# Kernel tuning notes

Measured on AMD Instinct MI355X. Metric: run time of the kernel, lower is better.

## Reference

```python
import jax, jax.numpy as jnp
import numpy as np

N = 50000      # nodes
E = 800000     # edges
D = 200        # in_dim = hid_dim
R = 230        # num_rels
B = 100        # bdd bases -> submat = D // B = 2
S = D // B     # submatrix size (2)


def setup_inputs() -> dict:
    key = jax.random.key(0)
    ks = jax.random.split(key, 16)
    node_feat = jax.random.normal(ks[0], (N, D), dtype=jnp.float32)
    dynamic_emb = jax.random.normal(ks[1], (N, 1, D), dtype=jnp.float32)
    src = jax.random.randint(ks[2], (E,), 0, N, dtype=jnp.int32)
    dst = jax.random.randint(ks[3], (E,), 0, N, dtype=jnp.int32)
    etypes = jax.random.randint(ks[4], (E,), 0, R, dtype=jnp.int32)
    # BDD relational weights per layer: [R, B, S, S]
    w1 = jax.random.normal(ks[5], (R, B, S, S), dtype=jnp.float32) * 0.1
    loop_w1 = jax.random.normal(ks[6], (D, D), dtype=jnp.float32) * 0.05
    b1 = jnp.zeros((D,), dtype=jnp.float32)
    w2 = jax.random.normal(ks[7], (R, B, S, S), dtype=jnp.float32) * 0.1
    loop_w2 = jax.random.normal(ks[8], (D, D), dtype=jnp.float32) * 0.05
    b2 = jnp.zeros((D,), dtype=jnp.float32)
    # single-layer vanilla RNN (tanh) params
    W_ih = jax.random.normal(ks[9], (D, D), dtype=jnp.float32) * 0.05
    W_hh = jax.random.normal(ks[10], (D, D), dtype=jnp.float32) * 0.05
    b_ih = jnp.zeros((D,), dtype=jnp.float32)
    b_hh = jnp.zeros((D,), dtype=jnp.float32)
    return {"node_feat": node_feat, "dynamic_emb": dynamic_emb,
            "src": src, "dst": dst, "etypes": etypes,
            "w1": w1, "loop_w1": loop_w1, "b1": b1,
            "w2": w2, "loop_w2": loop_w2, "b2": b2,
            "W_ih": W_ih, "W_hh": W_hh, "b_ih": b_ih, "b_hh": b_hh}


def _rel_graph_conv_bdd(x, src, dst, etypes, edge_norm, w, loop_w, b):
    # gather source feats and apply per-edge-type block-diagonal transform
    xs = x[src].reshape(E, B, S)                     # [E, B, S]
    msg = jnp.einsum('ebi,ebio->ebo', xs, w[etypes]) # [E, B, S]
    msg = msg.reshape(E, D) * edge_norm              # edge-norm scaling
    agg = jax.ops.segment_sum(msg, dst, num_segments=N)  # scatter-add to dst
    return agg + x @ loop_w + b                      # self-loop + bias


def reference(node_feat, dynamic_emb, src, dst, etypes,
              w1, loop_w1, b1, w2, loop_w2, b2,
              W_ih, W_hh, b_ih, b_hh):
    # edge_norm = dst node norm = 1 / in-degree
    deg = jax.ops.segment_sum(jnp.ones((E,), jnp.float32), dst, num_segments=N)
    node_norm = jnp.where(deg > 0, 1.0 / jnp.maximum(deg, 1.0), 0.0)
    edge_norm = node_norm[dst][:, None]              # [E, 1]

    # RGCN layer 1 (tanh activation), layer 2 (no activation); dropout=eval
    h = _rel_graph_conv_bdd(node_feat, src, dst, etypes, edge_norm, w1, loop_w1, b1)
    h = jnp.tanh(h)
    h = _rel_graph_conv_bdd(h, src, dst, etypes, edge_norm, w2, loop_w2, b2)

    # single-step vanilla RNN: hn = tanh(x W_ih^T + b_ih + h0 W_hh^T + b_hh)
    h0 = dynamic_emb[:, 0, :]                        # [N, D]
    hn = jnp.tanh(h @ W_ih.T + b_ih + h0 @ W_hh.T + b_hh)
    return hn[:, None, :]                            # [N, 1, D]
```

## Files before the change

kernel.cpp:

```cpp
#include <hip/hip_runtime.h>

#define N_NODES 50000
#define N_EDGES 800000
#define DIM     200
#define NBLK    100
#define NRELS   230
#define NB_SCAN 196
#define KPAD    224
#define KPN     256
#define NROWPAD 50048
#define NFRAG8  (8 * 14 * 64)
#define EPADMAX (N_EDGES + 3 * N_NODES + 16)
#define DUMMYROW 50000

typedef __attribute__((ext_vector_type(8)))  short short8;
typedef __attribute__((ext_vector_type(16))) float f32x16;

__device__ __forceinline__ unsigned short f2bf(float f) {
    unsigned u = __float_as_uint(f);
    u += 0x7fffu + ((u >> 16) & 1u);
    return (unsigned short)(u >> 16);
}

__device__ __forceinline__ float bflo(unsigned u) { return __uint_as_float(u << 16); }
__device__ __forceinline__ float bfhi(unsigned u) { return __uint_as_float(u & 0xffff0000u); }
__device__ __forceinline__ float b2f(unsigned short u) { return __uint_as_float((unsigned)u << 16); }

__device__ __forceinline__ float tanh_fast(float x) {
    float xa = fminf(fmaxf(x, -15.0f), 15.0f);
    float e = __expf(2.0f * xa);
    return (e - 1.0f) / (e + 1.0f);
}

__device__ __forceinline__ int uread(int v, int l) {
    return __builtin_amdgcn_readlane(v, l);
}

#if __has_builtin(__builtin_amdgcn_fdot2_f32_bf16)
typedef __bf16 bf16x2 __attribute__((ext_vector_type(2)));
__device__ __forceinline__ float dot2bf(unsigned a, unsigned b, float c) {
    return __builtin_amdgcn_fdot2_f32_bf16(
        __builtin_bit_cast(bf16x2, a), __builtin_bit_cast(bf16x2, b), c, false);
}
#define CMP4(XU, WU)                                                    \
    { m0 = dot2bf(XU.x, WU.x, m0); m1 = dot2bf(XU.x, WU.y, m1);         \
      m2 = dot2bf(XU.y, WU.z, m2); m3 = dot2bf(XU.y, WU.w, m3); }
#else
#define CMP4(XU, WU)                                                    \
    { float x0 = bflo(XU.x), x1 = bfhi(XU.x);                           \
      float x2 = bflo(XU.y), x3 = bfhi(XU.y);                           \
      m0 += x0 * bflo(WU.x) + x1 * bfhi(WU.x);                          \
      m1 += x0 * bflo(WU.y) + x1 * bfhi(WU.y);                          \
      m2 += x2 * bflo(WU.z) + x3 * bfhi(WU.z);                          \
      m3 += x2 * bflo(WU.w) + x3 * bfhi(WU.w); }
#endif

#define SWZ5(rr, off) ((unsigned)((rr) * 512 + (off)) ^ ((unsigned)((rr) & 15) << 4))

__global__ void deg_int_kernel(const int* __restrict__ dst, int* __restrict__ degi) {
    int e = blockIdx.x * blockDim.x + threadIdx.x;
    if (e < N_EDGES) atomicAdd(&degi[dst[e]], 1);
}

__global__ void prep_feat2(const float* __restrict__ x, const float* __restrict__ de,
                           unsigned short* __restrict__ xb, unsigned short* __restrict__ h0b) {
    const int HALF = NROWPAD * 28;
    int idx = blockIdx.x * blockDim.x + threadIdx.x;
    if (idx >= 2 * HALF) return;
    const float* src = (idx < HALF) ? x : de;
    unsigned short* o = (idx < HALF) ? xb : h0b;
    int j = (idx < HALF) ? idx : idx - HALF;
    int row = j / 28, c8 = j % 28;
    uint4 pk = {0, 0, 0, 0};
    if (row < N_NODES && c8 < 25) {
        const float* p = src + (size_t)row * DIM + c8 * 8;
        float4 a = *(const float4*)p;
        float4 b = *(const float4*)(p + 4);
        pk.x = (unsigned)f2bf(a.x) | ((unsigned)f2bf(a.y) << 16);
        pk.y = (unsigned)f2bf(a.z) | ((unsigned)f2bf(a.w) << 16);
        pk.z = (unsigned)f2bf(b.x) | ((unsigned)f2bf(b.y) << 16);
        pk.w = (unsigned)f2bf(b.z) | ((unsigned)f2bf(b.w) << 16);
    }
    *(uint4*)(o + (size_t)j * 8) = pk;
}

#define PS_C (2 * NRELS * NBLK)
#define PS_D (3 * NFRAG8)
#define PS_E ((DIM + 1) * DIM)
#define PS_TOTAL (PS_C + PS_D + PS_E)

__global__ __launch_bounds__(256) void prep_small(
        const float* __restrict__ w1, const float* __restrict__ w2,
        unsigned short* __restrict__ w1b, unsigned short* __restrict__ w2b,
        const float* __restrict__ lw1, const float* __restrict__ wih,
        const float* __restrict__ whh,
        unsigned short* __restrict__ w1f, unsigned short* __restrict__ wihf,
        unsigned short* __restrict__ whhf,
        const float* __restrict__ lw2, const float* __restrict__ b2,
        const float* __restrict__ b_ih, const float* __restrict__ b_hh,
        float* __restrict__ Mt) {
    int idx = blockIdx.x * blockDim.x + threadIdx.x;
    if (idx < PS_C) {
        const int HALF = NRELS * NBLK;
        const float* w = (idx < HALF) ? w1 : w2;
        unsigned short* o = (idx < HALF) ? w1b : w2b;
        int j = (idx < HALF) ? idx : idx - HALF;
        float4 v = *(const float4*)(w + (size_t)j * 4);
        unsigned c0 = (unsigned)f2bf(v.x) | ((unsigned)f2bf(v.z) << 16);
        unsigned c1 = (unsigned)f2bf(v.y) | ((unsigned)f2bf(v.w) << 16);
        *(uint2*)(o + (size_t)j * 4) = make_uint2(c0, c1);
        return;
    }
    idx -= PS_C;
    if (idx < PS_D) {
        int sec = idx / NFRAG8, f = idx % NFRAG8;
        const float* w = (sec == 0) ? lw1 : (sec == 1) ? wih : whh;
        unsigned short* o = (sec == 0) ? w1f : (sec == 1) ? wihf : whhf;
        int l = f & 63;
        int ks = (f >> 6) % 14;
        int nt = f / (14 * 64);
        int n  = nt * 32 + (l & 31);
        int k0 = ks * 16 + (l >> 5) * 8;
        unsigned short v[8];
        #pragma unroll
        for (int j = 0; j < 8; ++j) {
            int k = k0 + j;
            float val = 0.0f;
            if (n < DIM && k < DIM)
                val = (sec == 0) ? w[k * DIM + n] : w[n * DIM + k];
            v[j] = f2bf(val);
        }
        *(uint4*)(o + (size_t)f * 8) = *(uint4*)v;
        return;
    }
    idx -= PS_D;
    if (idx < PS_E) {
        int k = idx / DIM, n = idx % DIM;
        const float* ar = (k < DIM) ? (lw2 + (size_t)k * DIM) : b2;
        const float* br = wih + (size_t)n * DIM;
        float s0 = 0.f, s1 = 0.f, s2 = 0.f, s3 = 0.f;
        #pragma unroll 5
        for (int q = 0; q < DIM; q += 4) {
            float4 a = *(const float4*)(ar + q);
            float4 b = *(const float4*)(br + q);
            s0 += a.x * b.x; s1 += a.y * b.y; s2 += a.z * b.z; s3 += a.w * b.w;
        }
        float s = (s0 + s1) + (s2 + s3);
        if (k == DIM) s += b_ih[n] + b_hh[n];
        Mt[idx] = s;
    }
}

__global__ __launch_bounds__(256) void scanA(const int* __restrict__ degi,
                                             int* __restrict__ pos, int* __restrict__ cur,
                                             int* __restrict__ bsum) {
    __shared__ int tmp[256];
    int t = threadIdx.x;
    int g = blockIdx.x * 256 + t;
    int d = (g < N_NODES) ? degi[g] : 0;
    int v = (d + 3) & ~3;
    tmp[t] = v;
    __syncthreads();
    for (int off = 1; off < 256; off <<= 1) {
        int xv = (t >= off) ? tmp[t - off] : 0;
        __syncthreads();
        tmp[t] += xv;
        __syncthreads();
    }
    if (g < N_NODES) { int e = tmp[t] - v; pos[g] = e; cur[g] = e; }
    if (t == 255) bsum[blockIdx.x] = tmp[255];
}

__global__ __launch_bounds__(256) void scanC2(int* __restrict__ pos, int* __restrict__ cur,
                                              const int* __restrict__ bsum) {
    __shared__ int tmp[256];
    __shared__ int excl[256];
    int t = threadIdx.x;
    int v = (t < NB_SCAN) ? bsum[t] : 0;
    tmp[t] = v;
    __syncthreads();
    for (int off = 1; off < 256; off <<= 1) {
        int xv = (t >= off) ? tmp[t - off] : 0;
        __syncthreads();
        tmp[t] += xv;
        __syncthreads();
    }
    excl[t] = tmp[t] - v;
    __syncthreads();
    int add = excl[blockIdx.x];
    int g = blockIdx.x * 256 + t;
    if (g < N_NODES) { pos[g] += add; cur[g] += add; }
}

#define M2_A N_EDGES
#define M2_B N_NODES
#define M2_C (NFRAG8 + KPN)
#define M2_TOTAL (M2_A + M2_B + M2_C)

__global__ __launch_bounds__(256) void mega2(
        const int* __restrict__ src, const int* __restrict__ dst,
        const int* __restrict__ et,
        int* __restrict__ cur, const int* __restrict__ pos,
        const int* __restrict__ degi, int* __restrict__ se,
        const float* __restrict__ Mt, unsigned short* __restrict__ Mf,
        float* __restrict__ biasv) {
    int idx = blockIdx.x * blockDim.x + threadIdx.x;
    if (idx < M2_A) {
        int d = dst[idx];
        int slot = atomicAdd(&cur[d], 1);
        se[slot] = src[idx] | (et[idx] << 16);
        return;
    }
    idx -= M2_A;
    if (idx < M2_B) {
        int d = degi[idx];
        if (d > 0) {
            int dp = (d + 3) & ~3;
            int start = pos[idx];
            for (int j = d; j < dp; ++j) se[start + j] = DUMMYROW;
        }
        return;
    }
    idx -= M2_B;
    if (idx < NFRAG8) {
        int l = idx & 63;
        int ks = (idx >> 6) % 14;
        int nt = idx / (14 * 64);
        int n  = nt * 32 + (l & 31);
        int k0 = ks * 16 + (l >> 5) * 8;
        unsigned short v[8];
        #pragma unroll
        for (int j = 0; j < 8; ++j) {
            int k = k0 + j;
            v[j] = f2bf((n < DIM && k < DIM) ? Mt[k * DIM + n] : 0.0f);
        }
        *(uint4*)(Mf + (size_t)idx * 8) = *(uint4*)v;
    } else if (idx < NFRAG8 + KPN) {
        int n = idx - NFRAG8;
        biasv[n] = (n < DIM) ? Mt[DIM * DIM + n] : 0.0f;
    }
}

#define GL(QQ, XU, WU)                                                  \
    { int p_ = uread(sv, (QQ)); int s_ = p_ & 0xffff; int r_ = p_ >> 16;\
      XU = *(const uint2*)(x  + (size_t)s_ * KPAD + xoff);              \
      WU = *(const uint4*)(wb + (size_t)r_ * (NBLK * 4) + woff); }

__global__ __launch_bounds__(256) void gatherB(
        const unsigned short* __restrict__ x,
        const int*   __restrict__ se,
        const int*   __restrict__ pstart,
        const int*   __restrict__ degi,
        const unsigned short* __restrict__ wb,
        unsigned short* __restrict__ agg) {
    int node = (blockIdx.x * blockDim.x + threadIdx.x) >> 6;
    int lane = threadIdx.x & 63;
    if (node >= N_NODES) return;
    int deg = __builtin_amdgcn_readfirstlane(degi[node]);
    const bool act = (lane < 50);
    int cl   = act ? lane : 49;
    int xoff = 4 * cl;
    int woff = 8 * cl;

    if (deg == 0) {
        if (lane < 56) *(uint2*)(agg + (size_t)node * KPAD + 4 * lane) = make_uint2(0u, 0u);
        return;
    }
    int start = __builtin_amdgcn_readfirstlane(pstart[node]);
    int degp  = (deg + 3) & ~3;

    float m0 = 0.f, m1 = 0.f, m2 = 0.f, m3 = 0.f;

    for (int base = 0; base < degp; base += 64) {
        int cnt = degp - base; if (cnt > 64) cnt = 64;
        int sv = se[start + base + (lane < cnt ? lane : cnt - 1)];

        uint2 X0, X1, X2, X3, Y0, Y1, Y2, Y3;
        uint4 W0, W1, W2, W3, V0, V1, V2, V3;
        GL(0, X0, W0); GL(1, X1, W1); GL(2, X2, W2); GL(3, X3, W3);

        for (int q = 0; q < cnt; q += 8) {
            bool l1 = (q + 4 < cnt);
            if (l1) { GL(q + 4, Y0, V0); GL(q + 5, Y1, V1); GL(q + 6, Y2, V2); GL(q + 7, Y3, V3); }
            CMP4(X0, W0); CMP4(X1, W1); CMP4(X2, W2); CMP4(X3, W3);
            if (!l1) break;
            bool l2 = (q + 8 < cnt);
            if (l2) { GL(q + 8, X0, W0); GL(q + 9, X1, W1); GL(q + 10, X2, W2); GL(q + 11, X3, W3); }
            CMP4(Y0, V0); CMP4(Y1, V1); CMP4(Y2, V2); CMP4(Y3, V3);
        }
    }
    float nrm = 1.0f / (float)deg;
    uint2 ov = make_uint2(0u, 0u);
    if (act) {
        ov.x = (unsigned)f2bf(m0 * nrm) | ((unsigned)f2bf(m1 * nrm) << 16);
        ov.y = (unsigned)f2bf(m2 * nrm) | ((unsigned)f2bf(m3 * nrm) << 16);
    }
    if (lane < 56) *(uint2*)(agg + (size_t)node * KPAD + 4 * lane) = ov;
}

__global__ __launch_bounds__(256) void gemm1_kernel(
        unsigned short* xb_hb,
        const unsigned short* __restrict__ agg1,
        const float* __restrict__ b1,
        const unsigned short* __restrict__ w1f) {
    __shared__ __align__(16) unsigned short s_a[32 * KPN];
    int row0 = blockIdx.x * 32;
    int tid = threadIdx.x;
    for (int i = tid; i < 32 * 32; i += 256) {
        int rr = i >> 5, ch = i & 31;
        uint4 v = {0, 0, 0, 0};
        if (ch < 28) v = *(const uint4*)(xb_hb + (size_t)(row0 + rr) * KPAD + ch * 8);
        *(uint4*)((char*)s_a + SWZ5(rr, ch * 16)) = v;
    }
    __syncthreads();

    int l = tid & 63, wv = tid >> 6;
    int rl = l & 31, hl = l >> 5;
    int ntlo = wv * 2;
    const unsigned short* wb = w1f + (size_t)(ntlo * 14) * 512 + l * 8;

    f32x16 acc0 = {}, acc1 = {};
    short8 aC  = *(const short8*)((const char*)s_a + SWZ5(rl, (hl * 8) * 2));
    short8 b0C = *(const short8*)(wb);
    short8 b1C = *(const short8*)(wb + 14 * 512);
    #pragma unroll
    for (int ks = 0; ks < 13; ++ks) {
        short8 aN = {}, b0N = {}, b1N = {};
        if (ks < 12) {
            aN  = *(const short8*)((const char*)s_a + SWZ5(rl, ((ks + 1) * 16 + hl * 8) * 2));
            b0N = *(const short8*)(wb + (ks + 1) * 512);
            b1N = *(const short8*)(wb + 14 * 512 + (ks + 1) * 512);
        }
        acc0 = __builtin_amdgcn_mfma_f32_32x32x16_bf16(aC, b0C, acc0, 0, 0, 0);
        acc1 = __builtin_amdgcn_mfma_f32_32x32x16_bf16(aC, b1C, acc1, 0, 0, 0);
        aC = aN; b0C = b0N; b1C = b1N;
    }
    __syncthreads();

    #pragma unroll
    for (int t = 0; t < 2; ++t) {
        f32x16 ac = t ? acc1 : acc0;
        int gc = (ntlo + t) * 32 + rl;
        if (gc >= KPAD) continue;
        float bias = (gc < DIM) ? b1[gc] : 0.0f;
        #pragma unroll
        for (int r = 0; r < 16; ++r) {
            int gr = row0 + (r & 3) + 8 * (r >> 2) + 4 * hl;
            float v = 0.0f;
            if (gc < DIM && gr < N_NODES)
                v = ac[r] + b2f(agg1[(size_t)gr * KPAD + gc]) + bias;
            xb_hb[(size_t)gr * KPAD + gc] = f2bf(tanh_fast(v));
        }
    }
}

__global__ __launch_bounds__(256) void gemm2_kernel(
        const unsigned short* __restrict__ hb,
        const unsigned short* __restrict__ aggp,
        const unsigned short* __restrict__ h0b,
        const unsigned short* __restrict__ Mf,
        const unsigned short* __restrict__ wihf,
        const unsigned short* __restrict__ whhf,
        const float* __restrict__ biasv,
        float* __restrict__ out) {
    __shared__ __align__(16) unsigned short s_h[32 * KPN];
    __shared__ __align__(16) unsigned short s_g[32 * KPN];
    __shared__ __align__(16) unsigned short s_e[32 * KPN];
    int row0 = blockIdx.x * 32;
    int tid = threadIdx.x;
    for (int i = tid; i < 32 * 32; i += 256) {
        int rr = i >> 5, ch = i & 31;
        uint4 vh = {0,0,0,0}, vg = {0,0,0,0}, ve = {0,0,0,0};
        if (ch < 28) {
            size_t off = (size_t)(row0 + rr) * KPAD + ch * 8;
            vh = *(const uint4*)(hb   + off);
            vg = *(const uint4*)(aggp + off);
            ve = *(const uint4*)(h0b  + off);
        }
        unsigned sw = SWZ5(rr, ch * 16);
        *(uint4*)((char*)s_h + sw) = vh;
        *(uint4*)((char*)s_g + sw) = vg;
        *(uint4*)((char*)s_e + sw) = ve;
    }
    __syncthreads();

    int l = tid & 63, wv = tid >> 6;
    int rl = l & 31, hl = l >> 5;
    int ntlo = wv * 2;
    const unsigned short* pm = Mf   + (size_t)(ntlo * 14) * 512 + l * 8;
    const unsigned short* pi = wihf + (size_t)(ntlo * 14) * 512 + l * 8;
    const unsigned short* ph = whhf + (size_t)(ntlo * 14) * 512 + l * 8;

    f32x16 a0 = {}, a1 = {};
    unsigned off0 = SWZ5(rl, (hl * 8) * 2);
    short8 hC  = *(const short8*)((const char*)s_h + off0);
    short8 gC  = *(const short8*)((const char*)s_g + off0);
    short8 eC  = *(const short8*)((const char*)s_e + off0);
    short8 m0C = *(const short8*)(pm);
    short8 m1C = *(const short8*)(pm + 14 * 512);
    short8 i0C = *(const short8*)(pi);
    short8 i1C = *(const short8*)(pi + 14 * 512);
    short8 h0C = *(const short8*)(ph);
    short8 h1C = *(const short8*)(ph + 14 * 512);
    #pragma unroll
    for (int ks = 0; ks < 13; ++ks) {
        short8 hN = {}, gN = {}, eN = {};
        short8 m0N = {}, m1N = {}, i0N = {}, i1N = {}, h0N = {}, h1N = {};
        if (ks < 12) {
            unsigned off = SWZ5(rl, ((ks + 1) * 16 + hl * 8) * 2);
            hN  = *(const short8*)((const char*)s_h + off);
            gN  = *(const short8*)((const char*)s_g + off);
            eN  = *(const short8*)((const char*)s_e + off);
            m0N = *(const short8*)(pm + (ks + 1) * 512);
            m1N = *(const short8*)(pm + 14 * 512 + (ks + 1) * 512);
            i0N = *(const short8*)(pi + (ks + 1) * 512);
            i1N = *(const short8*)(pi + 14 * 512 + (ks + 1) * 512);
            h0N = *(const short8*)(ph + (ks + 1) * 512);
            h1N = *(const short8*)(ph + 14 * 512 + (ks + 1) * 512);
        }
        a0 = __builtin_amdgcn_mfma_f32_32x32x16_bf16(hC, m0C, a0, 0, 0, 0);
        a1 = __builtin_amdgcn_mfma_f32_32x32x16_bf16(hC, m1C, a1, 0, 0, 0);
        a0 = __builtin_amdgcn_mfma_f32_32x32x16_bf16(gC, i0C, a0, 0, 0, 0);
        a1 = __builtin_amdgcn_mfma_f32_32x32x16_bf16(gC, i1C, a1, 0, 0, 0);
        a0 = __builtin_amdgcn_mfma_f32_32x32x16_bf16(eC, h0C, a0, 0, 0, 0);
        a1 = __builtin_amdgcn_mfma_f32_32x32x16_bf16(eC, h1C, a1, 0, 0, 0);
        hC = hN; gC = gN; eC = eN;
        m0C = m0N; m1C = m1N; i0C = i0N; i1C = i1N; h0C = h0N; h1C = h1N;
    }

    #pragma unroll
    for (int t = 0; t < 2; ++t) {
        f32x16 oc = t ? a1 : a0;
        int gc = (ntlo + t) * 32 + rl;
        if (gc >= DIM) continue;
        float bias = biasv[gc];
        #pragma unroll
        for (int r = 0; r < 16; ++r) {
            int gr = row0 + (r & 3) + 8 * (r >> 2) + 4 * hl;
            if (gr < N_NODES)
                out[(size_t)gr * DIM + gc] = tanh_fast(oc[r] + bias);
        }
    }
}

extern "C" void kernel_launch(void* const* d_in, const int* in_sizes, int n_in,
                              void* d_out, int out_size, void* d_ws, size_t ws_size,
                              hipStream_t stream) {
    const float* node_feat = (const float*)d_in[0];
    const float* dyn_emb   = (const float*)d_in[1];
    const int*   src       = (const int*)  d_in[2];
    const int*   dst       = (const int*)  d_in[3];
    const int*   etypes    = (const int*)  d_in[4];
    const float* w1        = (const float*)d_in[5];
    const float* loop_w1   = (const float*)d_in[6];
    const float* b1        = (const float*)d_in[7];
    const float* w2        = (const float*)d_in[8];
    const float* loop_w2   = (const float*)d_in[9];
    const float* b2        = (const float*)d_in[10];
    const float* W_ih      = (const float*)d_in[11];
    const float* W_hh      = (const float*)d_in[12];
    const float* b_ih      = (const float*)d_in[13];
    const float* b_hh      = (const float*)d_in[14];
    float* out = (float*)d_out;

    int*   degi = (int*)d_ws;
    int*   pos  = degi + 51200;
    int*   cur  = pos  + 51200;
    int*   bsum = cur  + 51200;
    int*   se   = bsum + 256;
    unsigned short* aggp = (unsigned short*)(se + EPADMAX);
    unsigned short* hb   = aggp + (size_t)NROWPAD * KPAD;
    unsigned short* h0b  = hb   + (size_t)NROWPAD * KPAD;
    unsigned short* w1f  = h0b  + (size_t)NROWPAD * KPAD;
    unsigned short* wihf = w1f  + (size_t)NFRAG8 * 8;
    unsigned short* whhf = wihf + (size_t)NFRAG8 * 8;
    unsigned short* Mf   = whhf + (size_t)NFRAG8 * 8;
    unsigned short* w1b  = Mf   + (size_t)NFRAG8 * 8;
    unsigned short* w2b  = w1b  + (size_t)NRELS * NBLK * 4;
    float* biasv = (float*)(w2b + (size_t)NRELS * NBLK * 4);
    float* Mt    = biasv + KPN;

    hipMemsetAsync(degi, 0, 51200 * sizeof(int), stream);

    deg_int_kernel<<<(N_EDGES + 255) / 256, 256, 0, stream>>>(dst, degi);
    prep_feat2<<<(2 * NROWPAD * 28 + 255) / 256, 256, 0, stream>>>(
        node_feat, dyn_emb, hb, h0b);
    prep_small<<<(PS_TOTAL + 255) / 256, 256, 0, stream>>>(
        w1, w2, w1b, w2b, loop_w1, W_ih, W_hh, w1f, wihf, whhf,
        loop_w2, b2, b_ih, b_hh, Mt);

    scanA<<<NB_SCAN, 256, 0, stream>>>(degi, pos, cur, bsum);
    scanC2<<<NB_SCAN, 256, 0, stream>>>(pos, cur, bsum);

    mega2<<<(M2_TOTAL + 255) / 256, 256, 0, stream>>>(
        src, dst, etypes, cur, pos, degi, se, Mt, Mf, biasv);

    gatherB<<<(N_NODES * 64 + 255) / 256, 256, 0, stream>>>(
        hb, se, pos, degi, w1b, aggp);
    gemm1_kernel<<<(N_NODES + 31) / 32, 256, 0, stream>>>(
        hb, aggp, b1, w1f);

    gatherB<<<(N_NODES * 64 + 255) / 256, 256, 0, stream>>>(
        hb, se, pos, degi, w2b, aggp);

    gemm2_kernel<<<(N_NODES + 31) / 32, 256, 0, stream>>>(
        hb, aggp, h0b, Mf, wihf, whhf, biasv, out);
}
```

Measured before the change: 336.5 us.

## Fuse degree count into feature prep and halve gemm2 shared-memory staging

Merges the in-degree atomic kernel into the bf16 feature conversion kernel so one launch does both. In gemm2, the K dimension is now staged in two halves of 14 chunks each, cutting shared memory per block from 48KB to 24KB, with an extra barrier per half. The smaller LDS footprint is meant to let more blocks stay resident per CU. The cost is a second load/sync phase and the loss of overlap across the K split. The old loop's 13 k-steps covered K up to 208, while the new halves cover 7+7 steps (224), so padded zero columns are now also multiplied.

```diff
diff --git a/kernel.cpp b/kernel.cpp
--- a/kernel.cpp
+++ b/kernel.cpp
@@ -56,32 +56,37 @@
 #endif
 
 #define SWZ5(rr, off) ((unsigned)((rr) * 512 + (off)) ^ ((unsigned)((rr) & 15) << 4))
-
-__global__ void deg_int_kernel(const int* __restrict__ dst, int* __restrict__ degi) {
-    int e = blockIdx.x * blockDim.x + threadIdx.x;
-    if (e < N_EDGES) atomicAdd(&degi[dst[e]], 1);
-}
-
-__global__ void prep_feat2(const float* __restrict__ x, const float* __restrict__ de,
-                           unsigned short* __restrict__ xb, unsigned short* __restrict__ h0b) {
-    const int HALF = NROWPAD * 28;
+#define SWZH(rr, off) ((unsigned)((rr) * 256 + (off)) ^ ((unsigned)((rr) & 15) << 4))
+
+#define FD_A (2 * NROWPAD * 28)
+#define FD_B N_EDGES
+#define FD_TOTAL (FD_A + FD_B)
+
+__global__ void featdeg(const float* __restrict__ x, const float* __restrict__ de,
+                        unsigned short* __restrict__ xb, unsigned short* __restrict__ h0b,
+                        const int* __restrict__ dst, int* __restrict__ degi) {
     int idx = blockIdx.x * blockDim.x + threadIdx.x;
-    if (idx >= 2 * HALF) return;
-    const float* src = (idx < HALF) ? x : de;
-    unsigned short* o = (idx < HALF) ? xb : h0b;
-    int j = (idx < HALF) ? idx : idx - HALF;
-    int row = j / 28, c8 = j % 28;
-    uint4 pk = {0, 0, 0, 0};
-    if (row < N_NODES && c8 < 25) {
-        const float* p = src + (size_t)row * DIM + c8 * 8;
-        float4 a = *(const float4*)p;
-        float4 b = *(const float4*)(p + 4);
-        pk.x = (unsigned)f2bf(a.x) | ((unsigned)f2bf(a.y) << 16);
-        pk.y = (unsigned)f2bf(a.z) | ((unsigned)f2bf(a.w) << 16);
-        pk.z = (unsigned)f2bf(b.x) | ((unsigned)f2bf(b.y) << 16);
-        pk.w = (unsigned)f2bf(b.z) | ((unsigned)f2bf(b.w) << 16);
-    }
-    *(uint4*)(o + (size_t)j * 8) = pk;
+    if (idx < FD_A) {
+        const int HALF = NROWPAD * 28;
+        const float* src = (idx < HALF) ? x : de;
+        unsigned short* o = (idx < HALF) ? xb : h0b;
+        int j = (idx < HALF) ? idx : idx - HALF;
+        int row = j / 28, c8 = j % 28;
+        uint4 pk = {0, 0, 0, 0};
+        if (row < N_NODES && c8 < 25) {
+            const float* p = src + (size_t)row * DIM + c8 * 8;
+            float4 a = *(const float4*)p;
+            float4 b = *(const float4*)(p + 4);
+            pk.x = (unsigned)f2bf(a.x) | ((unsigned)f2bf(a.y) << 16);
+            pk.y = (unsigned)f2bf(a.z) | ((unsigned)f2bf(a.w) << 16);
+            pk.z = (unsigned)f2bf(b.x) | ((unsigned)f2bf(b.y) << 16);
+            pk.w = (unsigned)f2bf(b.z) | ((unsigned)f2bf(b.w) << 16);
+        }
+        *(uint4*)(o + (size_t)j * 8) = pk;
+        return;
+    }
+    idx -= FD_A;
+    if (idx < FD_B) atomicAdd(&degi[dst[idx]], 1);
 }
 
 #define PS_C (2 * NRELS * NBLK)
@@ -363,27 +368,11 @@
         const unsigned short* __restrict__ whhf,
         const float* __restrict__ biasv,
         float* __restrict__ out) {
-    __shared__ __align__(16) unsigned short s_h[32 * KPN];
-    __shared__ __align__(16) unsigned short s_g[32 * KPN];
-    __shared__ __align__(16) unsigned short s_e[32 * KPN];
+    __shared__ __align__(16) unsigned short s_h[32 * 128];
+    __shared__ __align__(16) unsigned short s_g[32 * 128];
+    __shared__ __align__(16) unsigned short s_e[32 * 128];
     int row0 = blockIdx.x * 32;
     int tid = threadIdx.x;
-    for (int i = tid; i < 32 * 32; i += 256) {
-        int rr = i >> 5, ch = i & 31;
-        uint4 vh = {0,0,0,0}, vg = {0,0,0,0}, ve = {0,0,0,0};
-        if (ch < 28) {
-            size_t off = (size_t)(row0 + rr) * KPAD + ch * 8;
-            vh = *(const uint4*)(hb   + off);
-            vg = *(const uint4*)(aggp + off);
-            ve = *(const uint4*)(h0b  + off);
-        }
-        unsigned sw = SWZ5(rr, ch * 16);
-        *(uint4*)((char*)s_h + sw) = vh;
-        *(uint4*)((char*)s_g + sw) = vg;
-        *(uint4*)((char*)s_e + sw) = ve;
-    }
-    __syncthreads();
-
     int l = tid & 63, wv = tid >> 6;
     int rl = l & 31, hl = l >> 5;
     int ntlo = wv * 2;
@@ -392,40 +381,56 @@
     const unsigned short* ph = whhf + (size_t)(ntlo * 14) * 512 + l * 8;
 
     f32x16 a0 = {}, a1 = {};
-    unsigned off0 = SWZ5(rl, (hl * 8) * 2);
-    short8 hC  = *(const short8*)((const char*)s_h + off0);
-    short8 gC  = *(const short8*)((const char*)s_g + off0);
-    short8 eC  = *(const short8*)((const char*)s_e + off0);
-    short8 m0C = *(const short8*)(pm);
-    short8 m1C = *(const short8*)(pm + 14 * 512);
-    short8 i0C = *(const short8*)(pi);
-    short8 i1C = *(const short8*)(pi + 14 * 512);
-    short8 h0C = *(const short8*)(ph);
-    short8 h1C = *(const short8*)(ph + 14 * 512);
-    #pragma unroll
-    for (int ks = 0; ks < 13; ++ks) {
-        short8 hN = {}, gN = {}, eN = {};
-        short8 m0N = {}, m1N = {}, i0N = {}, i1N = {}, h0N = {}, h1N = {};
-        if (ks < 12) {
-            unsigned off = SWZ5(rl, ((ks + 1) * 16 + hl * 8) * 2);
-            hN  = *(const short8*)((const char*)s_h + off);
-            gN  = *(const short8*)((const char*)s_g + off);
-            eN  = *(const short8*)((const char*)s_e + off);
-            m0N = *(const short8*)(pm + (ks + 1) * 512);
-            m1N = *(const short8*)(pm + 14 * 512 + (ks + 1) * 512);
-            i0N = *(const short8*)(pi + (ks + 1) * 512);
-            i1N = *(const short8*)(pi + 14 * 512 + (ks + 1) * 512);
-            h0N = *(const short8*)(ph + (ks + 1) * 512);
-            h1N = *(const short8*)(ph + 14 * 512 + (ks + 1) * 512);
-        }
-        a0 = __builtin_amdgcn_mfma_f32_32x32x16_bf16(hC, m0C, a0, 0, 0, 0);
-        a1 = __builtin_amdgcn_mfma_f32_32x32x16_bf16(hC, m1C, a1, 0, 0, 0);
-        a0 = __builtin_amdgcn_mfma_f32_32x32x16_bf16(gC, i0C, a0, 0, 0, 0);
-        a1 = __builtin_amdgcn_mfma_f32_32x32x16_bf16(gC, i1C, a1, 0, 0, 0);
-        a0 = __builtin_amdgcn_mfma_f32_32x32x16_bf16(eC, h0C, a0, 0, 0, 0);
-        a1 = __builtin_amdgcn_mfma_f32_32x32x16_bf16(eC, h1C, a1, 0, 0, 0);
-        hC = hN; gC = gN; eC = eN;
-        m0C = m0N; m1C = m1N; i0C = i0N; i1C = i1N; h0C = h0N; h1C = h1N;
+
+    for (int half = 0; half < 2; ++half) {
+        for (int i = tid; i < 32 * 14; i += 256) {
+            int rr = i / 14, ch = i % 14;
+            size_t off = (size_t)(row0 + rr) * KPAD + (half * 14 + ch) * 8;
+            unsigned sw = SWZH(rr, ch * 16);
+            *(uint4*)((char*)s_h + sw) = *(const uint4*)(hb   + off);
+            *(uint4*)((char*)s_g + sw) = *(const uint4*)(aggp + off);
+            *(uint4*)((char*)s_e + sw) = *(const uint4*)(h0b  + off);
+        }
+        __syncthreads();
+
+        const int kbase = half * 7;
+        unsigned off0 = SWZH(rl, (hl * 8) * 2);
+        short8 hC  = *(const short8*)((const char*)s_h + off0);
+        short8 gC  = *(const short8*)((const char*)s_g + off0);
+        short8 eC  = *(const short8*)((const char*)s_e + off0);
+        short8 m0C = *(const short8*)(pm + kbase * 512);
+        short8 m1C = *(const short8*)(pm + 14 * 512 + kbase * 512);
+        short8 i0C = *(const short8*)(pi + kbase * 512);
+        short8 i1C = *(const short8*)(pi + 14 * 512 + kbase * 512);
+        short8 h0C = *(const short8*)(ph + kbase * 512);
+        short8 h1C = *(const short8*)(ph + 14 * 512 + kbase * 512);
+        #pragma unroll
+        for (int ks = 0; ks < 7; ++ks) {
+            short8 hN = {}, gN = {}, eN = {};
+            short8 m0N = {}, m1N = {}, i0N = {}, i1N = {}, h0N = {}, h1N = {};
+            if (ks < 6) {
+                unsigned off = SWZH(rl, ((ks + 1) * 16 + hl * 8) * 2);
+                hN  = *(const short8*)((const char*)s_h + off);
+                gN  = *(const short8*)((const char*)s_g + off);
+                eN  = *(const short8*)((const char*)s_e + off);
+                int kg = kbase + ks + 1;
+                m0N = *(const short8*)(pm + kg * 512);
+                m1N = *(const short8*)(pm + 14 * 512 + kg * 512);
+                i0N = *(const short8*)(pi + kg * 512);
+                i1N = *(const short8*)(pi + 14 * 512 + kg * 512);
+                h0N = *(const short8*)(ph + kg * 512);
+                h1N = *(const short8*)(ph + 14 * 512 + kg * 512);
+            }
+            a0 = __builtin_amdgcn_mfma_f32_32x32x16_bf16(hC, m0C, a0, 0, 0, 0);
+            a1 = __builtin_amdgcn_mfma_f32_32x32x16_bf16(hC, m1C, a1, 0, 0, 0);
+            a0 = __builtin_amdgcn_mfma_f32_32x32x16_bf16(gC, i0C, a0, 0, 0, 0);
+            a1 = __builtin_amdgcn_mfma_f32_32x32x16_bf16(gC, i1C, a1, 0, 0, 0);
+            a0 = __builtin_amdgcn_mfma_f32_32x32x16_bf16(eC, h0C, a0, 0, 0, 0);
+            a1 = __builtin_amdgcn_mfma_f32_32x32x16_bf16(eC, h1C, a1, 0, 0, 0);
+            hC = hN; gC = gN; eC = eN;
+            m0C = m0N; m1C = m1N; i0C = i0N; i1C = i1N; h0C = h0N; h1C = h1N;
+        }
+        __syncthreads();
     }
 
     #pragma unroll
@@ -482,9 +487,8 @@
 
     hipMemsetAsync(degi, 0, 51200 * sizeof(int), stream);
 
-    deg_int_kernel<<<(N_EDGES + 255) / 256, 256, 0, stream>>>(dst, degi);
-    prep_feat2<<<(2 * NROWPAD * 28 + 255) / 256, 256, 0, stream>>>(
-        node_feat, dyn_emb, hb, h0b);
+    featdeg<<<(FD_TOTAL + 255) / 256, 256, 0, stream>>>(
+        node_feat, dyn_emb, hb, h0b, dst, degi);
     prep_small<<<(PS_TOTAL + 255) / 256, 256, 0, stream>>>(
         w1, w2, w1b, w2b, loop_w1, W_ih, W_hh, w1f, wihf, whhf,
         loop_w2, b2, b_ih, b_hh, Mt);
```

After: 333.5 us. About the same (-0.9%).
